# Kernel tuning notes

Measured on AMD Instinct MI355X. Metric: run time of the kernel, lower is better.

## Reference

```python
import jax, jax.numpy as jnp
import numpy as np

FACTOR = 2
GAIN = 1.0

def _setup_fir(fir=(1, 3, 3, 1), gain=GAIN):
    k = np.asarray(fir, dtype=np.float32)
    if k.ndim == 1:
        k = np.outer(k, k)
    k = k / k.sum() * gain
    return k  # (4, 4)

def setup_inputs() -> dict:
    key = jax.random.key(0)
    kx, kw = jax.random.split(key)
    N, C, H, W = 16, 320, 64, 64
    x = jax.random.normal(kx, (N, C, H, W), dtype=jnp.float32)
    # variance-scaling uniform init (DDPM style): fan_in = fan_out = C*9
    fan = C * 3 * 3
    bound = float(np.sqrt(3.0 / fan))
    w = jax.random.uniform(kw, (C, C, 3, 3), dtype=jnp.float32, minval=-bound, maxval=bound)
    fir_k = jnp.asarray(_setup_fir())
    return {"x": x, "w": w, "fir_k": fir_k}

def reference(x, w, fir_k):
    # Fused FIR (upfirdn2d with up=1, down=1) + strided 3x3 conv downsample.
    C = x.shape[1]
    convW = w.shape[3]          # 3
    kH = fir_k.shape[0]         # 4
    p = kH - FACTOR + (convW - 1)           # 4
    pad0, pad1 = (p + 1) // 2, p // 2       # (2, 2)
    # upfirdn2d: zero-pad then true convolution (flipped kernel), depthwise
    xp = jnp.pad(x, ((0, 0), (0, 0), (pad0, pad1), (pad0, pad1)))
    kf = jnp.flip(fir_k, (0, 1))            # symmetric here, kept for faithfulness
    kd = jnp.broadcast_to(kf[None, None], (C, 1, kH, kH))
    y = jax.lax.conv_general_dilated(
        xp, kd, window_strides=(1, 1), padding='VALID',
        dimension_numbers=('NCHW', 'OIHW', 'NCHW'), feature_group_count=C)
    # strided conv2d, padding=0, stride=factor
    out = jax.lax.conv_general_dilated(
        y, w, window_strides=(FACTOR, FACTOR), padding='VALID',
        dimension_numbers=('NCHW', 'OIHW', 'NCHW'))
    return out  # [N, C, H//2, W//2]
```

## Files before the change

kernel.cpp:

```cpp
#include <hip/hip_runtime.h>
#include <hip/hip_bf16.h>


typedef short bf16x8_t __attribute__((ext_vector_type(8)));
typedef float f32x4 __attribute__((ext_vector_type(4)));
typedef unsigned int u32x4 __attribute__((ext_vector_type(4)));
typedef __attribute__((address_space(1))) const unsigned int* as1_u32p;
typedef __attribute__((address_space(3))) unsigned int* as3_u32p;

#define NI 16
#define CCH 320
#define HW 64
#define HY 65
#define HY2 4225
#define CCSTEP 135200

__global__ __launch_bounds__(256) void fir_kernel(const float* __restrict__ x,
                                                  const float* __restrict__ fir_k,
                                                  __hip_bfloat16* __restrict__ yt) {
    __shared__ float vlds[8 * 16 * 69];
    int bx = blockIdx.x;
    int n   = bx / 180;
    int rr  = bx % 180;
    int r0  = (rr / 20) * 8;
    int ci0 = (rr % 20) * 16;

    float f0 = fir_k[0] + fir_k[1] + fir_k[2] + fir_k[3];
    float f1 = fir_k[4] + fir_k[5] + fir_k[6] + fir_k[7];
    float f2 = fir_k[8] + fir_k[9] + fir_k[10] + fir_k[11];
    float f3 = fir_k[12] + fir_k[13] + fir_k[14] + fir_k[15];

    int tid = threadIdx.x;
    int lane = tid & 63;
    int g = tid >> 6;

    for (int cis = g; cis < 16; cis += 4) {
        int ci = ci0 + cis;
        const float* xb = x + (size_t)(n * CCH + ci) * HW * HW;
        float xr[11];
#pragma unroll
        for (int jr = 0; jr < 11; ++jr) {
            int row = r0 + jr - 2;
            xr[jr] = (row >= 0 && row < HW) ? xb[row * HW + lane] : 0.f;
        }
#pragma unroll
        for (int j = 0; j < 8; ++j) {
            float v = f0 * xr[j] + f1 * xr[j + 1] + f2 * xr[j + 2] + f3 * xr[j + 3];
            float* vrow = vlds + (j * 16 + cis) * 69;
            vrow[lane + 2] = v;
            if (lane < 2)   vrow[lane] = 0.f;
            if (lane >= 62) vrow[lane + 4] = 0.f;
        }
    }
    __syncthreads();

    unsigned short* yu = (unsigned short*)yt;
#pragma unroll
    for (int i = 0; i < 4; ++i) {
        int slot = 4 * i + g;
        int j = slot >> 1, oct = slot & 1;
        int r = r0 + j;
        if (r >= HY) continue;
        int qg = (rr % 20) * 2 + oct;
        size_t obase = ((size_t)(n * 40 + qg) * HY2 + (size_t)r * HY) * 8;
        const float* vb = vlds + (j * 16 + oct * 8) * 69;
        int nc = (lane == 63) ? 2 : 1;
        for (int e = 0; e < nc; ++e) {
            int c = lane + e;
            float a[8];
#pragma unroll
            for (int u = 0; u < 8; ++u) {
                const float* vr = vb + u * 69 + c;
                a[u] = f0 * vr[0] + f1 * vr[1] + f2 * vr[2] + f3 * vr[3];
            }
            unsigned int wd[4];
#pragma unroll
            for (int h = 0; h < 4; ++h) {
                unsigned int lo = __bfloat16_as_ushort(__float2bfloat16(a[2 * h]));
                unsigned int hi = __bfloat16_as_ushort(__float2bfloat16(a[2 * h + 1]));
                wd[h] = lo | (hi << 16);
            }
            *(u32x4*)(yu + obase + (size_t)c * 8) = (u32x4){wd[0], wd[1], wd[2], wd[3]};
        }
    }
}

__global__ __launch_bounds__(256) void wt2_kernel(const float* __restrict__ w,
                                                  __hip_bfloat16* __restrict__ wt) {
    int idx = blockIdx.x * 256 + threadIdx.x;
    if (idx < 9 * CCH * CCH) {
        int j  = idx & 7;
        int co = (idx >> 3) % CCH;
        int t2 = idx / 2560;
        int q  = t2 & 3;
        int cc = (t2 >> 2) % 10;
        int tap = t2 / 40;
        int ci = cc * 32 + q * 8 + j;
        wt[idx] = __float2bfloat16(w[(co * CCH + ci) * 9 + tap]);
    }
}

__global__ __launch_bounds__(256, 3) void conv_kernel(const __hip_bfloat16* __restrict__ yt,
                                                      const __hip_bfloat16* __restrict__ wt2,
                                                      float* __restrict__ out) {
    __shared__ short ylds[2][1536 * 8];

    int bx = blockIdx.x;
    int sp = bx & 15;
    int t  = bx >> 4;
    int cb = t % 5;
    int n  = t / 5;
    int co0 = cb * 64;
    int oh0 = (sp >> 1) * 4;
    int ow0 = (sp & 1) * 16;

    int tid = threadIdx.x;
    int lane = tid & 63;
    int wid = tid >> 6;
    int q = lane >> 4, lc = lane & 15;

    const unsigned short* ytu = (const unsigned short*)yt;
    const unsigned short* wtu = (const unsigned short*)wt2;

    int ybase = n * 40 * HY2 * 8 + ((2 * oh0) * HY + 2 * ow0) * 8;
    int goff[6];
#pragma unroll
    for (int k = 0; k < 6; ++k) {
        int u = k * 256 + tid;
        int uc = (u < 1485) ? u : 1484;
        int p = uc / 5, s = uc - p * 5;
        if (s == 4) s = 3;
        int pr = p / 33, pc = p - pr * 33;
        goff[k] = ybase + (s * HY2 + pr * HY + pc) * 8;
    }

    const unsigned short* wbl = wtu + q * 2560 + (size_t)(co0 + wid * 16 + lc) * 8;
    const int aoff = (2 * lc) * 40 + q * 8;

    f32x4 acc[4];
#pragma unroll
    for (int i = 0; i < 4; ++i) acc[i] = (f32x4){0.f, 0.f, 0.f, 0.f};

    bf16x8_t bfr[2][9];

#define GLDS(buf, K, ccidx)                                                            \
    __builtin_amdgcn_global_load_lds(                                                  \
        (as1_u32p)(ytu + goff[K] + (ccidx) * CCSTEP),                                  \
        (as3_u32p)(&ylds[buf][(size_t)((K) * 256 + wid * 64) * 8]), 16, 0, 0)

#pragma unroll
    for (int k = 0; k < 6; ++k) GLDS(0, k, 0);
#pragma unroll
    for (int kk = 0; kk < 9; ++kk)
        bfr[0][kk] = *(const bf16x8_t*)(wbl + kk * 102400);
    __syncthreads();

    auto compute = [&](const short* buf, const bf16x8_t* b) {
#pragma unroll
        for (int kw = 0; kw < 3; ++kw) {
            bf16x8_t af[9];
#pragma unroll
            for (int r = 0; r < 9; ++r)
                af[r] = *(const bf16x8_t*)(buf + aoff + (r * 33 + kw) * 40);
#pragma unroll
            for (int kh = 0; kh < 3; ++kh)
#pragma unroll
                for (int mf = 0; mf < 4; ++mf)
                    acc[mf] = __builtin_amdgcn_mfma_f32_16x16x32_bf16(
                        b[kh * 3 + kw], af[2 * mf + kh], acc[mf], 0, 0, 0);
        }
    };

    for (int tt = 0; tt < 5; ++tt) {
        int cc0 = 2 * tt, cc1 = 2 * tt + 1;
        {
#pragma unroll
            for (int k = 0; k < 6; ++k) GLDS(1, k, cc0 + 1);
            const unsigned short* wnx = wbl + (cc0 + 1) * 10240;
#pragma unroll
            for (int kk = 0; kk < 9; ++kk)
                bfr[1][kk] = *(const bf16x8_t*)(wnx + kk * 102400);
            compute(&ylds[0][0], bfr[0]);
            __syncthreads();
        }
        {
            if (cc1 < 9) {
#pragma unroll
                for (int k = 0; k < 6; ++k) GLDS(0, k, cc1 + 1);
                const unsigned short* wnx = wbl + (cc1 + 1) * 10240;
#pragma unroll
                for (int kk = 0; kk < 9; ++kk)
                    bfr[0][kk] = *(const bf16x8_t*)(wnx + kk * 102400);
            }
            compute(&ylds[1][0], bfr[1]);
            if (cc1 < 9) __syncthreads();
        }
    }
#undef GLDS

#pragma unroll
    for (int mf = 0; mf < 4; ++mf) {
        int oh = oh0 + mf;
        int ow = ow0 + lc;
#pragma unroll
        for (int rg = 0; rg < 4; ++rg) {
            int co = co0 + wid * 16 + q * 4 + rg;
            out[((n * CCH + co) * 32 + oh) * 32 + ow] = acc[mf][rg];
        }
    }
}

__global__ __launch_bounds__(256) void naive_kernel(const float* __restrict__ x,
                                                    const float* __restrict__ w,
                                                    const float* __restrict__ fk,
                                                    float* __restrict__ out) {
    int idx = blockIdx.x * 256 + threadIdx.x;
    if (idx >= NI * CCH * 32 * 32) return;
    int ow = idx & 31;
    int oh = (idx >> 5) & 31;
    int co = (idx >> 10) % CCH;
    int n = (idx >> 10) / CCH;
    float f0 = fk[0] + fk[1] + fk[2] + fk[3];
    float f1 = fk[4] + fk[5] + fk[6] + fk[7];
    float f2 = fk[8] + fk[9] + fk[10] + fk[11];
    float f3 = fk[12] + fk[13] + fk[14] + fk[15];
    float fv[4] = {f0, f1, f2, f3};
    float acc = 0.f;
    for (int ci = 0; ci < CCH; ++ci) {
        const float* xb = x + (size_t)(n * CCH + ci) * HW * HW;
        const float* wb = w + (size_t)(co * CCH + ci) * 9;
#pragma unroll
        for (int u = 0; u < 3; ++u) {
            int yr = 2 * oh + u;
#pragma unroll
            for (int v = 0; v < 3; ++v) {
                int yc = 2 * ow + v;
                float s = 0.f;
#pragma unroll
                for (int a = 0; a < 4; ++a) {
                    int xrw = yr - 2 + a;
                    if (xrw < 0 || xrw >= HW) continue;
                    float t = 0.f;
#pragma unroll
                    for (int b = 0; b < 4; ++b) {
                        int xc = yc - 2 + b;
                        if (xc >= 0 && xc < HW) t += fv[b] * xb[xrw * HW + xc];
                    }
                    s += fv[a] * t;
                }
                acc += wb[u * 3 + v] * s;
            }
        }
    }
    out[idx] = acc;
}

extern "C" void kernel_launch(void* const* d_in, const int* in_sizes, int n_in,
                              void* d_out, int out_size, void* d_ws, size_t ws_size,
                              hipStream_t stream) {
    const float* x = (const float*)d_in[0];
    const float* w = (const float*)d_in[1];
    const float* fk = (const float*)d_in[2];
    float* out = (float*)d_out;

    const size_t ybytes = (size_t)NI * 40 * HY2 * 8 * 2;
    const size_t wtoff = ybytes;
    const size_t need = wtoff + (size_t)9 * CCH * CCH * 2;

    if (ws_size >= need) {
        __hip_bfloat16* yt = (__hip_bfloat16*)d_ws;
        __hip_bfloat16* wt = (__hip_bfloat16*)((char*)d_ws + wtoff);
        fir_kernel<<<16 * 9 * 20, 256, 0, stream>>>(x, fk, yt);
        wt2_kernel<<<(9 * CCH * CCH + 255) / 256, 256, 0, stream>>>(w, wt);
        conv_kernel<<<16 * 5 * 16, 256, 0, stream>>>(yt, wt, out);
    } else {
        naive_kernel<<<(NI * CCH * 32 * 32 + 255) / 256, 256, 0, stream>>>(x, w, fk, out);
    }
}
```

Baseline: 78.93 us.

## Interleave four channel octets per pixel in bf16 intermediate layout

Changes the FIR output tensor layout from [n][40 octets][pixel][8] to [n][10 chunks][pixel][32], so each pixel holds 32 contiguous channels. The FIR store loop now has lanes alternate between octets and write adjacent 16-byte pieces, and the last column is handled by a separate small tail. The conv kernel's global-to-LDS gather offsets are updated so the four octet loads for a pixel land in one contiguous 64-byte span. The goal is better coalescing and fewer DRAM pages touched on the conv input loads and the FIR stores, with CCSTEP still used for stepping chunks.

```diff
diff --git a/kernel.cpp b/kernel.cpp
--- a/kernel.cpp
+++ b/kernel.cpp
@@ -23,7 +23,8 @@
     int n   = bx / 180;
     int rr  = bx % 180;
     int r0  = (rr / 20) * 8;
-    int ci0 = (rr % 20) * 16;
+    int cig = rr % 20;
+    int ci0 = cig * 16;
 
     float f0 = fir_k[0] + fir_k[1] + fir_k[2] + fir_k[3];
     float f1 = fir_k[4] + fir_k[5] + fir_k[6] + fir_k[7];
@@ -54,23 +55,45 @@
     }
     __syncthreads();
 
+    int cc = cig >> 1;
+    int O  = (cig & 1) * 2;
     unsigned short* yu = (unsigned short*)yt;
+    int oct = lane & 1;
+    int cl  = lane >> 1;
+    size_t pbase = (size_t)(n * 10 + cc) * HY2;
 #pragma unroll
     for (int i = 0; i < 4; ++i) {
         int slot = 4 * i + g;
-        int j = slot >> 1, oct = slot & 1;
+        int j = slot >> 1, half = slot & 1;
         int r = r0 + j;
         if (r >= HY) continue;
-        int qg = (rr % 20) * 2 + oct;
-        size_t obase = ((size_t)(n * 40 + qg) * HY2 + (size_t)r * HY) * 8;
-        const float* vb = vlds + (j * 16 + oct * 8) * 69;
-        int nc = (lane == 63) ? 2 : 1;
-        for (int e = 0; e < nc; ++e) {
-            int c = lane + e;
+        int c = half * 32 + cl;
+        const float* vb = vlds + (j * 16 + oct * 8) * 69 + c;
+        float a[8];
+#pragma unroll
+        for (int u = 0; u < 8; ++u) {
+            const float* vr = vb + u * 69;
+            a[u] = f0 * vr[0] + f1 * vr[1] + f2 * vr[2] + f3 * vr[3];
+        }
+        unsigned int wd[4];
+#pragma unroll
+        for (int h = 0; h < 4; ++h) {
+            unsigned int lo = __bfloat16_as_ushort(__float2bfloat16(a[2 * h]));
+            unsigned int hi = __bfloat16_as_ushort(__float2bfloat16(a[2 * h + 1]));
+            wd[h] = lo | (hi << 16);
+        }
+        *(u32x4*)(yu + (pbase + (size_t)r * HY + c) * 32 + (O + oct) * 8) =
+            (u32x4){wd[0], wd[1], wd[2], wd[3]};
+    }
+    if (tid < 16) {
+        int j = tid >> 1, oc2 = tid & 1;
+        int r = r0 + j;
+        if (r < HY) {
+            const float* vb = vlds + (j * 16 + oc2 * 8) * 69 + 64;
             float a[8];
 #pragma unroll
             for (int u = 0; u < 8; ++u) {
-                const float* vr = vb + u * 69 + c;
+                const float* vr = vb + u * 69;
                 a[u] = f0 * vr[0] + f1 * vr[1] + f2 * vr[2] + f3 * vr[3];
             }
             unsigned int wd[4];
@@ -80,7 +103,8 @@
                 unsigned int hi = __bfloat16_as_ushort(__float2bfloat16(a[2 * h + 1]));
                 wd[h] = lo | (hi << 16);
             }
-            *(u32x4*)(yu + obase + (size_t)c * 8) = (u32x4){wd[0], wd[1], wd[2], wd[3]};
+            *(u32x4*)(yu + (pbase + (size_t)r * HY + 64) * 32 + (O + oc2) * 8) =
+                (u32x4){wd[0], wd[1], wd[2], wd[3]};
         }
     }
 }
@@ -122,7 +146,7 @@
     const unsigned short* ytu = (const unsigned short*)yt;
     const unsigned short* wtu = (const unsigned short*)wt2;
 
-    int ybase = n * 40 * HY2 * 8 + ((2 * oh0) * HY + 2 * ow0) * 8;
+    int ybase = (n * 10 * HY2 + (2 * oh0) * HY + 2 * ow0) * 32;
     int goff[6];
 #pragma unroll
     for (int k = 0; k < 6; ++k) {
@@ -131,7 +155,7 @@
         int p = uc / 5, s = uc - p * 5;
         if (s == 4) s = 3;
         int pr = p / 33, pc = p - pr * 33;
-        goff[k] = ybase + (s * HY2 + pr * HY + pc) * 8;
+        goff[k] = ybase + (pr * HY + pc) * 32 + s * 8;
     }
 
     const unsigned short* wbl = wtu + q * 2560 + (size_t)(co0 + wid * 16 + lc) * 8;
@@ -263,7 +287,7 @@
     const float* fk = (const float*)d_in[2];
     float* out = (float*)d_out;
 
-    const size_t ybytes = (size_t)NI * 40 * HY2 * 8 * 2;
+    const size_t ybytes = (size_t)NI * 10 * HY2 * 32 * 2;
     const size_t wtoff = ybytes;
     const size_t need = wtoff + (size_t)9 * CCH * CCH * 2;
 
```

New measurement: 77.64 us. About the same (-1.6%).

## Interleave 32-channel groups in FIR output layout and retile FIR kernel

Applied to the files above, without the earlier changes.

Changes the intermediate bf16 FIR output layout from 8-channel groups stored as separate planes to 32-channel groups interleaved per pixel. Each conv load then reads 64 contiguous bytes per pixel instead of four strided 16-byte chunks. The FIR kernel is retiled to 4 rows by 32 channels per block so it writes the new layout with coalesced stores. The conv kernel's gather offsets are updated to match, and the channel-step stride CCSTEP is left unchanged, which may be wrong for the new layout.

```diff
diff --git a/kernel.cpp b/kernel.cpp
--- a/kernel.cpp
+++ b/kernel.cpp
@@ -18,12 +18,13 @@
 __global__ __launch_bounds__(256) void fir_kernel(const float* __restrict__ x,
                                                   const float* __restrict__ fir_k,
                                                   __hip_bfloat16* __restrict__ yt) {
-    __shared__ float vlds[8 * 16 * 69];
+    __shared__ float vlds[4 * 32 * 69];
     int bx = blockIdx.x;
-    int n   = bx / 180;
-    int rr  = bx % 180;
-    int r0  = (rr / 20) * 8;
-    int ci0 = (rr % 20) * 16;
+    int n    = bx / 170;
+    int rem  = bx % 170;
+    int band = rem / 10;
+    int cc   = rem % 10;
+    int r0   = band * 4;
 
     float f0 = fir_k[0] + fir_k[1] + fir_k[2] + fir_k[3];
     float f1 = fir_k[4] + fir_k[5] + fir_k[6] + fir_k[7];
@@ -34,19 +35,19 @@
     int lane = tid & 63;
     int g = tid >> 6;
 
-    for (int cis = g; cis < 16; cis += 4) {
-        int ci = ci0 + cis;
+    for (int cis = g; cis < 32; cis += 4) {
+        int ci = cc * 32 + cis;
         const float* xb = x + (size_t)(n * CCH + ci) * HW * HW;
-        float xr[11];
-#pragma unroll
-        for (int jr = 0; jr < 11; ++jr) {
-            int row = r0 + jr - 2;
-            xr[jr] = (row >= 0 && row < HW) ? xb[row * HW + lane] : 0.f;
-        }
-#pragma unroll
-        for (int j = 0; j < 8; ++j) {
+        float xr[7];
+#pragma unroll
+        for (int t = 0; t < 7; ++t) {
+            int row = r0 + t - 2;
+            xr[t] = (row >= 0 && row < HW) ? xb[row * HW + lane] : 0.f;
+        }
+#pragma unroll
+        for (int j = 0; j < 4; ++j) {
             float v = f0 * xr[j] + f1 * xr[j + 1] + f2 * xr[j + 2] + f3 * xr[j + 3];
-            float* vrow = vlds + (j * 16 + cis) * 69;
+            float* vrow = vlds + (j * 32 + cis) * 69;
             vrow[lane + 2] = v;
             if (lane < 2)   vrow[lane] = 0.f;
             if (lane >= 62) vrow[lane + 4] = 0.f;
@@ -55,32 +56,34 @@
     __syncthreads();
 
     unsigned short* yu = (unsigned short*)yt;
-#pragma unroll
-    for (int i = 0; i < 4; ++i) {
-        int slot = 4 * i + g;
-        int j = slot >> 1, oct = slot & 1;
-        int r = r0 + j;
-        if (r >= HY) continue;
-        int qg = (rr % 20) * 2 + oct;
-        size_t obase = ((size_t)(n * 40 + qg) * HY2 + (size_t)r * HY) * 8;
-        const float* vb = vlds + (j * 16 + oct * 8) * 69;
-        int nc = (lane == 63) ? 2 : 1;
-        for (int e = 0; e < nc; ++e) {
-            int c = lane + e;
-            float a[8];
-#pragma unroll
-            for (int u = 0; u < 8; ++u) {
-                const float* vr = vb + u * 69 + c;
-                a[u] = f0 * vr[0] + f1 * vr[1] + f2 * vr[2] + f3 * vr[3];
+    int s  = tid & 3;
+    int pl = tid >> 2;
+    size_t plane = (size_t)(n * 10 + cc) * HY2;
+#pragma unroll
+    for (int it = 0; it < 5; ++it) {
+        int pid = it * 64 + pl;
+        if (pid < 260) {
+            int j = pid / 65;
+            int c = pid % 65;
+            int r = r0 + j;
+            if (r < HY) {
+                const float* vb = vlds + (j * 32 + s * 8) * 69 + c;
+                float a[8];
+#pragma unroll
+                for (int k = 0; k < 8; ++k) {
+                    const float* vr = vb + k * 69;
+                    a[k] = f0 * vr[0] + f1 * vr[1] + f2 * vr[2] + f3 * vr[3];
+                }
+                unsigned int wd[4];
+#pragma unroll
+                for (int h = 0; h < 4; ++h) {
+                    unsigned int lo = __bfloat16_as_ushort(__float2bfloat16(a[2 * h]));
+                    unsigned int hi = __bfloat16_as_ushort(__float2bfloat16(a[2 * h + 1]));
+                    wd[h] = lo | (hi << 16);
+                }
+                *(u32x4*)(yu + (plane + (size_t)r * HY + c) * 32 + s * 8) =
+                    (u32x4){wd[0], wd[1], wd[2], wd[3]};
             }
-            unsigned int wd[4];
-#pragma unroll
-            for (int h = 0; h < 4; ++h) {
-                unsigned int lo = __bfloat16_as_ushort(__float2bfloat16(a[2 * h]));
-                unsigned int hi = __bfloat16_as_ushort(__float2bfloat16(a[2 * h + 1]));
-                wd[h] = lo | (hi << 16);
-            }
-            *(u32x4*)(yu + obase + (size_t)c * 8) = (u32x4){wd[0], wd[1], wd[2], wd[3]};
         }
     }
 }
@@ -122,7 +125,7 @@
     const unsigned short* ytu = (const unsigned short*)yt;
     const unsigned short* wtu = (const unsigned short*)wt2;
 
-    int ybase = n * 40 * HY2 * 8 + ((2 * oh0) * HY + 2 * ow0) * 8;
+    int ybase = (n * 10 * HY2 + (2 * oh0) * HY + 2 * ow0) * 32;
     int goff[6];
 #pragma unroll
     for (int k = 0; k < 6; ++k) {
@@ -131,7 +134,7 @@
         int p = uc / 5, s = uc - p * 5;
         if (s == 4) s = 3;
         int pr = p / 33, pc = p - pr * 33;
-        goff[k] = ybase + (s * HY2 + pr * HY + pc) * 8;
+        goff[k] = ybase + (pr * HY + pc) * 32 + s * 8;
     }
 
     const unsigned short* wbl = wtu + q * 2560 + (size_t)(co0 + wid * 16 + lc) * 8;
@@ -263,14 +266,14 @@
     const float* fk = (const float*)d_in[2];
     float* out = (float*)d_out;
 
-    const size_t ybytes = (size_t)NI * 40 * HY2 * 8 * 2;
+    const size_t ybytes = (size_t)NI * 10 * HY2 * 32 * 2;
     const size_t wtoff = ybytes;
     const size_t need = wtoff + (size_t)9 * CCH * CCH * 2;
 
     if (ws_size >= need) {
         __hip_bfloat16* yt = (__hip_bfloat16*)d_ws;
         __hip_bfloat16* wt = (__hip_bfloat16*)((char*)d_ws + wtoff);
-        fir_kernel<<<16 * 9 * 20, 256, 0, stream>>>(x, fk, yt);
+        fir_kernel<<<16 * 17 * 10, 256, 0, stream>>>(x, fk, yt);
         wt2_kernel<<<(9 * CCH * CCH + 255) / 256, 256, 0, stream>>>(w, wt);
         conv_kernel<<<16 * 5 * 16, 256, 0, stream>>>(yt, wt, out);
     } else {
```

After: 76.42 us. 1.03x faster.
